# Kernel optimization log

Measured on AMD Instinct MI355X. Metric: run time of the kernel, lower is better.

## Reference

```python
import jax, jax.numpy as jnp
import numpy as np

E = 8        # num_experts
TOP_K = 2    # num_experts_per_tok
H = 2048     # hidden_size
I = 1408     # moe_intermediate_size

def setup_inputs() -> dict:
    key = jax.random.key(0)
    k0, k1, k2, k3, k4 = jax.random.split(key, 5)
    hidden_states = jax.random.normal(k0, (2, 2048, H), dtype=jnp.float32)
    gate_w = jax.random.normal(k1, (E, H), dtype=jnp.float32) * 0.02   # router: Linear(H, E)
    wg = jax.random.normal(k2, (E, I, H), dtype=jnp.float32) * 0.02    # gate_proj per expert
    wu = jax.random.normal(k3, (E, I, H), dtype=jnp.float32) * 0.02    # up_proj per expert
    wd = jax.random.normal(k4, (E, H, I), dtype=jnp.float32) * 0.02    # down_proj per expert
    return {"hidden_states": hidden_states, "gate_w": gate_w, "wg": wg, "wu": wu, "wd": wd}

def reference(hidden_states, gate_w, wg, wu, wd):
    b, s, h = hidden_states.shape
    x = hidden_states.reshape(-1, h)                      # [T, H]
    router_logits = x @ gate_w.T                          # [T, E]
    routing_weights = jax.nn.softmax(router_logits.astype(jnp.float32), axis=-1)
    topk_weight, topk_idx = jax.lax.top_k(routing_weights, TOP_K)   # [T, K]
    topk_weight = topk_weight / jnp.sum(topk_weight, axis=-1, keepdims=True)
    # per-token combine weight for each expert: w[t,e] = sum_k topk_weight[t,k] * [topk_idx[t,k]==e]
    comb = jnp.sum(jax.nn.one_hot(topk_idx, E, dtype=x.dtype) * topk_weight[..., None].astype(x.dtype), axis=1)  # [T, E]
    # compute each expert on all tokens (dense faithful equivalent of masked dispatch), combine with comb
    def expert_out(e):
        g = x @ wg[e].T                                   # [T, I]
        u = x @ wu[e].T                                   # [T, I]
        return (jax.nn.silu(g) * u) @ wd[e].T             # [T, H]
    y = jnp.zeros_like(x)
    for e in range(E):  # small fixed expert count
        y = y + expert_out(e) * comb[:, e:e+1]
    final = y.reshape(b, s, h)
    return final, router_logits.astype(hidden_states.dtype)
```

## Files before the change

kernel.cpp:

```cpp
#include <hip/hip_runtime.h>

#define NTOK 4096
#define NEXP 8
#define HD 2048
#define ID 1408

typedef unsigned short u16;
typedef __attribute__((ext_vector_type(8))) short short8;
typedef __attribute__((ext_vector_type(4))) float f32x4;
typedef const __attribute__((address_space(1))) void* gas_ptr;
typedef __attribute__((address_space(3))) void* las_ptr;

__device__ __forceinline__ u16 f2bf(float f) {
  unsigned int u = __float_as_uint(f);
  u += 0x7FFFu + ((u >> 16) & 1u);
  return (u16)(u >> 16);
}

__device__ __forceinline__ void async16(const u16* g, u16* l) {
  __builtin_amdgcn_global_load_lds((gas_ptr)g, (las_ptr)l, 16, 0, 0);
}

__global__ void cvt_kernel(const float* __restrict__ s, u16* __restrict__ d, long n8) {
  long i = (long)blockIdx.x * blockDim.x + threadIdx.x;
  if (i >= n8) return;
  const float4* s4 = (const float4*)s;
  float4 a = s4[2*i], b = s4[2*i+1];
  short8 o;
  o[0] = (short)f2bf(a.x); o[1] = (short)f2bf(a.y);
  o[2] = (short)f2bf(a.z); o[3] = (short)f2bf(a.w);
  o[4] = (short)f2bf(b.x); o[5] = (short)f2bf(b.y);
  o[6] = (short)f2bf(b.z); o[7] = (short)f2bf(b.w);
  *(short8*)(d + 8*i) = o;
}

__global__ void router_kernel(const float* __restrict__ x, const float* __restrict__ gw,
                              float* __restrict__ logits, int* __restrict__ cnt,
                              int* __restrict__ ptok, float* __restrict__ pw) {
  int t = blockIdx.x * 4 + (threadIdx.x >> 6);
  int lane = threadIdx.x & 63;
  if (t >= NTOK) return;
  const float4* xr = (const float4*)(x + (size_t)t * HD);
  float dot[NEXP];
#pragma unroll
  for (int e = 0; e < NEXP; ++e) dot[e] = 0.f;
#pragma unroll
  for (int c = 0; c < 8; ++c) {
    float4 xv = xr[c*64 + lane];
#pragma unroll
    for (int e = 0; e < NEXP; ++e) {
      float4 gv = ((const float4*)(gw + e*HD))[c*64 + lane];
      dot[e] += xv.x*gv.x + xv.y*gv.y + xv.z*gv.z + xv.w*gv.w;
    }
  }
#pragma unroll
  for (int off = 32; off > 0; off >>= 1) {
#pragma unroll
    for (int e = 0; e < NEXP; ++e) dot[e] += __shfl_xor(dot[e], off);
  }
  if (lane < NEXP) logits[(size_t)t*NEXP + lane] = dot[lane];
  if (lane == 0) {
    float mx = dot[0];
#pragma unroll
    for (int e = 1; e < NEXP; ++e) mx = fmaxf(mx, dot[e]);
    float p[NEXP];
#pragma unroll
    for (int e = 0; e < NEXP; ++e) p[e] = __expf(dot[e] - mx);
    int e0 = 0;
#pragma unroll
    for (int e = 1; e < NEXP; ++e) if (p[e] > p[e0]) e0 = e;
    int e1 = (e0 == 0) ? 1 : 0;
#pragma unroll
    for (int e = 0; e < NEXP; ++e) if (e != e0 && p[e] > p[e1]) e1 = e;
    float denom = p[e0] + p[e1];
    int pos0 = atomicAdd(&cnt[e0], 1);
    ptok[e0*NTOK + pos0] = t; pw[e0*NTOK + pos0] = p[e0] / denom;
    int pos1 = atomicAdd(&cnt[e1], 1);
    ptok[e1*NTOK + pos1] = t; pw[e1*NTOK + pos1] = p[e1] / denom;
  }
}

__global__ void prefix_kernel(const int* __restrict__ cnt, int* __restrict__ offs) {
  if (threadIdx.x == 0) {
    int a = 0;
    for (int e = 0; e < NEXP; ++e) { offs[e] = a; a += cnt[e]; }
  }
}

__global__ __launch_bounds__(256, 2) void gemm1_kernel(
    const u16* __restrict__ xb, const u16* __restrict__ wgb, const u16* __restrict__ wub,
    const int* __restrict__ cnt, const int* __restrict__ offs,
    const int* __restrict__ ptok, u16* __restrict__ hbuf) {
  int e = blockIdx.z, mt = blockIdx.y, nt = blockIdx.x;
  int c = cnt[e];
  if (mt * 128 >= c) return;
  int off = offs[e];

  __shared__ u16 sA[128*32], sBg[128*32], sBu[128*32];

  int tid = threadIdx.x;
  int r0 = tid >> 2;
  int ch = (tid & 3) * 8;
  int s0 = mt*128 + r0, s1 = s0 + 64;
  int t0 = ptok[e*NTOK + (s0 < c ? s0 : 0)];
  int t1 = ptok[e*NTOK + (s1 < c ? s1 : 0)];
  const u16* ga0 = xb + (size_t)t0*HD + ch;
  const u16* ga1 = xb + (size_t)t1*HD + ch;
  int n0 = nt*128 + r0;
  const u16* gg0 = wgb + ((size_t)e*ID + n0)*HD + ch;
  const u16* gg1 = gg0 + (size_t)64*HD;
  const u16* gu0 = wub + ((size_t)e*ID + n0)*HD + ch;
  const u16* gu1 = gu0 + (size_t)64*HD;

  int lane = tid & 63, wv = tid >> 6, wr = wv >> 1, wc = wv & 1;
  int fm = lane & 15, kg = lane >> 4;

  f32x4 accg[4][4], accu[4][4];
#pragma unroll
  for (int i = 0; i < 4; ++i)
#pragma unroll
    for (int j = 0; j < 4; ++j) {
      accg[i][j] = {0.f, 0.f, 0.f, 0.f};
      accu[i][j] = {0.f, 0.f, 0.f, 0.f};
    }

  const u16* sAf  = sA  + (wr*64 + fm)*32 + kg*8;
  const u16* sBgf = sBg + (wc*64 + fm)*32 + kg*8;
  const u16* sBuf = sBu + (wc*64 + fm)*32 + kg*8;

  for (int k0 = 0; k0 < HD; k0 += 32) {
    async16(ga0 + k0, sA + tid*8);
    async16(ga1 + k0, sA + 2048 + tid*8);
    async16(gg0 + k0, sBg + tid*8);
    async16(gg1 + k0, sBg + 2048 + tid*8);
    async16(gu0 + k0, sBu + tid*8);
    async16(gu1 + k0, sBu + 2048 + tid*8);
    __syncthreads();
    short8 af[4], bg[4], bu[4];
#pragma unroll
    for (int i = 0; i < 4; ++i) af[i] = *(const short8*)(sAf + i*512);
#pragma unroll
    for (int j = 0; j < 4; ++j) {
      bg[j] = *(const short8*)(sBgf + j*512);
      bu[j] = *(const short8*)(sBuf + j*512);
    }
#pragma unroll
    for (int i = 0; i < 4; ++i)
#pragma unroll
      for (int j = 0; j < 4; ++j) {
        accg[i][j] = __builtin_amdgcn_mfma_f32_16x16x32_bf16(af[i], bg[j], accg[i][j], 0, 0, 0);
        accu[i][j] = __builtin_amdgcn_mfma_f32_16x16x32_bf16(af[i], bu[j], accu[i][j], 0, 0, 0);
      }
    __syncthreads();
  }

#pragma unroll
  for (int i = 0; i < 4; ++i) {
#pragma unroll
    for (int r = 0; r < 4; ++r) {
      int slot = mt*128 + wr*64 + i*16 + kg*4 + r;
      if (slot < c) {
        size_t rowb = (size_t)(off + slot) * ID + nt*128 + wc*64 + fm;
#pragma unroll
        for (int j = 0; j < 4; ++j) {
          float g = accg[i][j][r], u = accu[i][j][r];
          float hh = g * u / (1.f + __expf(-g));
          hbuf[rowb + (size_t)j*16] = f2bf(hh);
        }
      }
    }
  }
}

__global__ __launch_bounds__(256, 2) void gemm2_kernel(
    const u16* __restrict__ hbuf, const u16* __restrict__ wdb,
    const int* __restrict__ cnt, const int* __restrict__ offs,
    const int* __restrict__ ptok, const float* __restrict__ pw,
    float* __restrict__ out) {
  int e = blockIdx.z, mt = blockIdx.y, nt = blockIdx.x;
  int c = cnt[e];
  if (mt * 128 >= c) return;
  int off = offs[e];

  __shared__ u16 sA[128*32], sB[128*32];

  int tid = threadIdx.x;
  int r0 = tid >> 2;
  int ch = (tid & 3) * 8;
  int s0 = mt*128 + r0, s1 = s0 + 64;
  const u16* ga0 = hbuf + (size_t)(off + (s0 < c ? s0 : 0))*ID + ch;
  const u16* ga1 = hbuf + (size_t)(off + (s1 < c ? s1 : 0))*ID + ch;
  int n0 = nt*128 + r0;
  const u16* gb0 = wdb + ((size_t)e*HD + n0)*ID + ch;
  const u16* gb1 = gb0 + (size_t)64*ID;

  int lane = tid & 63, wv = tid >> 6, wr = wv >> 1, wc = wv & 1;
  int fm = lane & 15, kg = lane >> 4;

  f32x4 acc[4][4];
#pragma unroll
  for (int i = 0; i < 4; ++i)
#pragma unroll
    for (int j = 0; j < 4; ++j) acc[i][j] = {0.f, 0.f, 0.f, 0.f};

  const u16* sAf = sA + (wr*64 + fm)*32 + kg*8;
  const u16* sBf = sB + (wc*64 + fm)*32 + kg*8;

  for (int k0 = 0; k0 < ID; k0 += 32) {
    async16(ga0 + k0, sA + tid*8);
    async16(ga1 + k0, sA + 2048 + tid*8);
    async16(gb0 + k0, sB + tid*8);
    async16(gb1 + k0, sB + 2048 + tid*8);
    __syncthreads();
    short8 af[4], bf[4];
#pragma unroll
    for (int i = 0; i < 4; ++i) af[i] = *(const short8*)(sAf + i*512);
#pragma unroll
    for (int j = 0; j < 4; ++j) bf[j] = *(const short8*)(sBf + j*512);
#pragma unroll
    for (int i = 0; i < 4; ++i)
#pragma unroll
      for (int j = 0; j < 4; ++j)
        acc[i][j] = __builtin_amdgcn_mfma_f32_16x16x32_bf16(af[i], bf[j], acc[i][j], 0, 0, 0);
    __syncthreads();
  }

#pragma unroll
  for (int i = 0; i < 4; ++i) {
#pragma unroll
    for (int r = 0; r < 4; ++r) {
      int slot = mt*128 + wr*64 + i*16 + kg*4 + r;
      if (slot < c) {
        int tok = ptok[e*NTOK + slot];
        float wgt = pw[e*NTOK + slot];
        float* orow = out + (size_t)tok*HD + nt*128 + wc*64 + fm;
#pragma unroll
        for (int j = 0; j < 4; ++j)
          atomicAdd(orow + j*16, wgt * acc[i][j][r]);
      }
    }
  }
}

extern "C" void kernel_launch(void* const* d_in, const int* in_sizes, int n_in,
                              void* d_out, int out_size, void* d_ws, size_t ws_size,
                              hipStream_t stream) {
  const float* x  = (const float*)d_in[0];
  const float* gw = (const float*)d_in[1];
  const float* wg = (const float*)d_in[2];
  const float* wu = (const float*)d_in[3];
  const float* wd = (const float*)d_in[4];
  float* out = (float*)d_out;

  char* p = (char*)d_ws;
  u16*   xb   = (u16*)(p);
  u16*   wgb  = (u16*)(p + 16777216UL);
  u16*   wub  = (u16*)(p + 62914560UL);
  u16*   wdb  = (u16*)(p + 109051904UL);
  u16*   hbuf = (u16*)(p + 155189248UL);
  int*   ptok = (int*)(p + 178257920UL);
  float* pww  = (float*)(p + 178388992UL);
  int*   cnt  = (int*)(p + 178520064UL);
  int*   offs = (int*)(p + 178520320UL);

  hipMemsetAsync(out, 0, (size_t)NTOK * HD * sizeof(float), stream);
  hipMemsetAsync(cnt, 0, NEXP * sizeof(int), stream);

  cvt_kernel<<<4096, 256, 0, stream>>>(x, xb, (long)NTOK * HD / 8);
  cvt_kernel<<<11264, 256, 0, stream>>>(wg, wgb, (long)NEXP * ID * HD / 8);
  cvt_kernel<<<11264, 256, 0, stream>>>(wu, wub, (long)NEXP * ID * HD / 8);
  cvt_kernel<<<11264, 256, 0, stream>>>(wd, wdb, (long)NEXP * HD * ID / 8);

  router_kernel<<<1024, 256, 0, stream>>>(x, gw, out + (size_t)NTOK * HD, cnt, ptok, pww);
  prefix_kernel<<<1, 64, 0, stream>>>(cnt, offs);

  gemm1_kernel<<<dim3(11, 32, 8), 256, 0, stream>>>(xb, wgb, wub, cnt, offs, ptok, hbuf);
  gemm2_kernel<<<dim3(16, 32, 8), 256, 0, stream>>>(hbuf, wdb, cnt, offs, ptok, pww, out);
}
```

Before: 695.6 us.

## Double-buffer GEMM LDS tiles, remap blocks per XCD, fuse x conversion into router

Both expert GEMMs now use two LDS buffers, so the async global-to-LDS load of the next K-slice is issued before the MFMAs on the current slice. The grid is flattened and block indices are remapped so that all N-tiles of a given (expert, M-tile) land on the same XCD, which should improve L2 reuse of the gathered activation rows. The separate fp32-to-bf16 conversion of x is folded into the router kernel, saving one launch and one extra read of x. The cost is double the LDS per block, which may limit occupancy, particularly for gemm1's three tile arrays.

After: 737.3 us. 6.0% more time.

```diff
diff --git a/kernel.cpp b/kernel.cpp
--- a/kernel.cpp
+++ b/kernel.cpp
@@ -7,6 +7,7 @@
 
 typedef unsigned short u16;
 typedef __attribute__((ext_vector_type(8))) short short8;
+typedef __attribute__((ext_vector_type(4))) short short4v;
 typedef __attribute__((ext_vector_type(4))) float f32x4;
 typedef const __attribute__((address_space(1))) void* gas_ptr;
 typedef __attribute__((address_space(3))) void* las_ptr;
@@ -35,18 +36,24 @@
 }
 
 __global__ void router_kernel(const float* __restrict__ x, const float* __restrict__ gw,
+                              u16* __restrict__ xb,
                               float* __restrict__ logits, int* __restrict__ cnt,
                               int* __restrict__ ptok, float* __restrict__ pw) {
   int t = blockIdx.x * 4 + (threadIdx.x >> 6);
   int lane = threadIdx.x & 63;
   if (t >= NTOK) return;
   const float4* xr = (const float4*)(x + (size_t)t * HD);
+  u16* xbr = xb + (size_t)t * HD;
   float dot[NEXP];
 #pragma unroll
   for (int e = 0; e < NEXP; ++e) dot[e] = 0.f;
 #pragma unroll
   for (int c = 0; c < 8; ++c) {
     float4 xv = xr[c*64 + lane];
+    short4v o;
+    o[0] = (short)f2bf(xv.x); o[1] = (short)f2bf(xv.y);
+    o[2] = (short)f2bf(xv.z); o[3] = (short)f2bf(xv.w);
+    *(short4v*)(xbr + (c*64 + lane)*4) = o;
 #pragma unroll
     for (int e = 0; e < NEXP; ++e) {
       float4 gv = ((const float4*)(gw + e*HD))[c*64 + lane];
@@ -91,12 +98,17 @@
     const u16* __restrict__ xb, const u16* __restrict__ wgb, const u16* __restrict__ wub,
     const int* __restrict__ cnt, const int* __restrict__ offs,
     const int* __restrict__ ptok, u16* __restrict__ hbuf) {
-  int e = blockIdx.z, mt = blockIdx.y, nt = blockIdx.x;
+  int b = blockIdx.x;
+  int xcd = b & 7;
+  int j = b >> 3;
+  int gidx = j / 11, nt = j % 11;
+  int g = gidx * 8 + xcd;
+  int e = g >> 5, mt = g & 31;
   int c = cnt[e];
   if (mt * 128 >= c) return;
   int off = offs[e];
 
-  __shared__ u16 sA[128*32], sBg[128*32], sBu[128*32];
+  __shared__ u16 sA[2][128*32], sBg[2][128*32], sBu[2][128*32];
 
   int tid = threadIdx.x;
   int r0 = tid >> 2;
@@ -119,40 +131,51 @@
 #pragma unroll
   for (int i = 0; i < 4; ++i)
 #pragma unroll
-    for (int j = 0; j < 4; ++j) {
-      accg[i][j] = {0.f, 0.f, 0.f, 0.f};
-      accu[i][j] = {0.f, 0.f, 0.f, 0.f};
-    }
-
-  const u16* sAf  = sA  + (wr*64 + fm)*32 + kg*8;
-  const u16* sBgf = sBg + (wc*64 + fm)*32 + kg*8;
-  const u16* sBuf = sBu + (wc*64 + fm)*32 + kg*8;
-
+    for (int jj = 0; jj < 4; ++jj) {
+      accg[i][jj] = {0.f, 0.f, 0.f, 0.f};
+      accu[i][jj] = {0.f, 0.f, 0.f, 0.f};
+    }
+
+  const int aoff = (wr*64 + fm)*32 + kg*8;
+  const int boff = (wc*64 + fm)*32 + kg*8;
+
+#define STAGE1(buf, k0) do { \
+    async16(ga0 + (k0), sA[buf] + tid*8); \
+    async16(ga1 + (k0), sA[buf] + 2048 + tid*8); \
+    async16(gg0 + (k0), sBg[buf] + tid*8); \
+    async16(gg1 + (k0), sBg[buf] + 2048 + tid*8); \
+    async16(gu0 + (k0), sBu[buf] + tid*8); \
+    async16(gu1 + (k0), sBu[buf] + 2048 + tid*8); \
+  } while (0)
+
+  STAGE1(0, 0);
+  __syncthreads();
+  int cur = 0;
   for (int k0 = 0; k0 < HD; k0 += 32) {
-    async16(ga0 + k0, sA + tid*8);
-    async16(ga1 + k0, sA + 2048 + tid*8);
-    async16(gg0 + k0, sBg + tid*8);
-    async16(gg1 + k0, sBg + 2048 + tid*8);
-    async16(gu0 + k0, sBu + tid*8);
-    async16(gu1 + k0, sBu + 2048 + tid*8);
-    __syncthreads();
+    int nk = k0 + 32;
+    if (nk < HD) STAGE1(cur ^ 1, nk);
+    const u16* pa = sA[cur] + aoff;
+    const u16* pg = sBg[cur] + boff;
+    const u16* pu = sBu[cur] + boff;
     short8 af[4], bg[4], bu[4];
 #pragma unroll
-    for (int i = 0; i < 4; ++i) af[i] = *(const short8*)(sAf + i*512);
-#pragma unroll
-    for (int j = 0; j < 4; ++j) {
-      bg[j] = *(const short8*)(sBgf + j*512);
-      bu[j] = *(const short8*)(sBuf + j*512);
+    for (int i = 0; i < 4; ++i) af[i] = *(const short8*)(pa + i*512);
+#pragma unroll
+    for (int jj = 0; jj < 4; ++jj) {
+      bg[jj] = *(const short8*)(pg + jj*512);
+      bu[jj] = *(const short8*)(pu + jj*512);
     }
 #pragma unroll
     for (int i = 0; i < 4; ++i)
 #pragma unroll
-      for (int j = 0; j < 4; ++j) {
-        accg[i][j] = __builtin_amdgcn_mfma_f32_16x16x32_bf16(af[i], bg[j], accg[i][j], 0, 0, 0);
-        accu[i][j] = __builtin_amdgcn_mfma_f32_16x16x32_bf16(af[i], bu[j], accu[i][j], 0, 0, 0);
+      for (int jj = 0; jj < 4; ++jj) {
+        accg[i][jj] = __builtin_amdgcn_mfma_f32_16x16x32_bf16(af[i], bg[jj], accg[i][jj], 0, 0, 0);
+        accu[i][jj] = __builtin_amdgcn_mfma_f32_16x16x32_bf16(af[i], bu[jj], accu[i][jj], 0, 0, 0);
       }
     __syncthreads();
-  }
+    cur ^= 1;
+  }
+#undef STAGE1
 
 #pragma unroll
   for (int i = 0; i < 4; ++i) {
@@ -162,10 +185,10 @@
       if (slot < c) {
         size_t rowb = (size_t)(off + slot) * ID + nt*128 + wc*64 + fm;
 #pragma unroll
-        for (int j = 0; j < 4; ++j) {
-          float g = accg[i][j][r], u = accu[i][j][r];
-          float hh = g * u / (1.f + __expf(-g));
-          hbuf[rowb + (size_t)j*16] = f2bf(hh);
+        for (int jj = 0; jj < 4; ++jj) {
+          float gg = accg[i][jj][r], uu = accu[i][jj][r];
+          float hh = gg * uu / (1.f + __expf(-gg));
+          hbuf[rowb + (size_t)jj*16] = f2bf(hh);
         }
       }
     }
@@ -177,12 +200,17 @@
     const int* __restrict__ cnt, const int* __restrict__ offs,
     const int* __restrict__ ptok, const float* __restrict__ pw,
     float* __restrict__ out) {
-  int e = blockIdx.z, mt = blockIdx.y, nt = blockIdx.x;
+  int b = blockIdx.x;
+  int xcd = b & 7;
+  int j = b >> 3;
+  int gidx = j >> 4, nt = j & 15;
+  int g = gidx * 8 + xcd;
+  int e = g >> 5, mt = g & 31;
   int c = cnt[e];
   if (mt * 128 >= c) return;
   int off = offs[e];
 
-  __shared__ u16 sA[128*32], sB[128*32];
+  __shared__ u16 sA[2][128*32], sB[2][128*32];
 
   int tid = threadIdx.x;
   int r0 = tid >> 2;
@@ -201,29 +229,40 @@
 #pragma unroll
   for (int i = 0; i < 4; ++i)
 #pragma unroll
-    for (int j = 0; j < 4; ++j) acc[i][j] = {0.f, 0.f, 0.f, 0.f};
-
-  const u16* sAf = sA + (wr*64 + fm)*32 + kg*8;
-  const u16* sBf = sB + (wc*64 + fm)*32 + kg*8;
-
+    for (int jj = 0; jj < 4; ++jj) acc[i][jj] = {0.f, 0.f, 0.f, 0.f};
+
+  const int aoff = (wr*64 + fm)*32 + kg*8;
+  const int boff = (wc*64 + fm)*32 + kg*8;
+
+#define STAGE2(buf, k0) do { \
+    async16(ga0 + (k0), sA[buf] + tid*8); \
+    async16(ga1 + (k0), sA[buf] + 2048 + tid*8); \
+    async16(gb0 + (k0), sB[buf] + tid*8); \
+    async16(gb1 + (k0), sB[buf] + 2048 + tid*8); \
+  } while (0)
+
+  STAGE2(0, 0);
+  __syncthreads();
+  int cur = 0;
   for (int k0 = 0; k0 < ID; k0 += 32) {
-    async16(ga0 + k0, sA + tid*8);
-    async16(ga1 + k0, sA + 2048 + tid*8);
-    async16(gb0 + k0, sB + tid*8);
-    async16(gb1 + k0, sB + 2048 + tid*8);
+    int nk = k0 + 32;
+    if (nk < ID) STAGE2(cur ^ 1, nk);
+    const u16* pa = sA[cur] + aoff;
+    const u16* pb = sB[cur] + boff;
+    short8 af[4], bf[4];
+#pragma unroll
+    for (int i = 0; i < 4; ++i) af[i] = *(const short8*)(pa + i*512);
+#pragma unroll
+    for (int jj = 0; jj < 4; ++jj) bf[jj] = *(const short8*)(pb + jj*512);
+#pragma unroll
+    for (int i = 0; i < 4; ++i)
+#pragma unroll
+      for (int jj = 0; jj < 4; ++jj)
+        acc[i][jj] = __builtin_amdgcn_mfma_f32_16x16x32_bf16(af[i], bf[jj], acc[i][jj], 0, 0, 0);
     __syncthreads();
-    short8 af[4], bf[4];
-#pragma unroll
-    for (int i = 0; i < 4; ++i) af[i] = *(const short8*)(sAf + i*512);
-#pragma unroll
-    for (int j = 0; j < 4; ++j) bf[j] = *(const short8*)(sBf + j*512);
-#pragma unroll
-    for (int i = 0; i < 4; ++i)
-#pragma unroll
-      for (int j = 0; j < 4; ++j)
-        acc[i][j] = __builtin_amdgcn_mfma_f32_16x16x32_bf16(af[i], bf[j], acc[i][j], 0, 0, 0);
-    __syncthreads();
-  }
+    cur ^= 1;
+  }
+#undef STAGE2
 
 #pragma unroll
   for (int i = 0; i < 4; ++i) {
@@ -235,8 +274,8 @@
         float wgt = pw[e*NTOK + slot];
         float* orow = out + (size_t)tok*HD + nt*128 + wc*64 + fm;
 #pragma unroll
-        for (int j = 0; j < 4; ++j)
-          atomicAdd(orow + j*16, wgt * acc[i][j][r]);
+        for (int jj = 0; jj < 4; ++jj)
+          atomicAdd(orow + jj*16, wgt * acc[i][jj][r]);
       }
     }
   }
@@ -266,14 +305,13 @@
   hipMemsetAsync(out, 0, (size_t)NTOK * HD * sizeof(float), stream);
   hipMemsetAsync(cnt, 0, NEXP * sizeof(int), stream);
 
-  cvt_kernel<<<4096, 256, 0, stream>>>(x, xb, (long)NTOK * HD / 8);
   cvt_kernel<<<11264, 256, 0, stream>>>(wg, wgb, (long)NEXP * ID * HD / 8);
   cvt_kernel<<<11264, 256, 0, stream>>>(wu, wub, (long)NEXP * ID * HD / 8);
   cvt_kernel<<<11264, 256, 0, stream>>>(wd, wdb, (long)NEXP * HD * ID / 8);
 
-  router_kernel<<<1024, 256, 0, stream>>>(x, gw, out + (size_t)NTOK * HD, cnt, ptok, pww);
+  router_kernel<<<1024, 256, 0, stream>>>(x, gw, xb, out + (size_t)NTOK * HD, cnt, ptok, pww);
   prefix_kernel<<<1, 64, 0, stream>>>(cnt, offs);
 
-  gemm1_kernel<<<dim3(11, 32, 8), 256, 0, stream>>>(xb, wgb, wub, cnt, offs, ptok, hbuf);
-  gemm2_kernel<<<dim3(16, 32, 8), 256, 0, stream>>>(hbuf, wdb, cnt, offs, ptok, pww, out);
-}
+  gemm1_kernel<<<2816, 256, 0, stream>>>(xb, wgb, wub, cnt, offs, ptok, hbuf);
+  gemm2_kernel<<<4096, 256, 0, stream>>>(hbuf, wdb, cnt, offs, ptok, pww, out);
+}
```
